# Kernel tuning notes

Hardware: AMD Instinct MI355X
Metric: run time of the kernel (lower is better)

The kernel has to match this reference:

```python
import jax, jax.numpy as jnp
import numpy as np

B, D, NB, BS = 32, 2048, 16, 512  # batch, dim_input=dim_output, n_blocks, block_size; NB*BS*BS == D*D


def setup_inputs() -> dict:
    key = jax.random.key(0)
    k1, k2, k3, k4, k5 = jax.random.split(key, 5)
    x = jax.random.normal(k1, (B, D), dtype=jnp.float32)
    gate_w = jax.random.normal(k2, (D, NB), dtype=jnp.float32) / np.sqrt(D)
    gate_b = jax.random.normal(k3, (NB,), dtype=jnp.float32) * 0.02
    weight = jax.random.normal(k4, (D, D), dtype=jnp.float32) / np.sqrt(D)  # kaiming-uniform-like scale
    bias = jax.random.normal(k5, (D,), dtype=jnp.float32) * (1.0 / np.sqrt(D))
    return {"x": x, "gate_w": gate_w, "gate_b": gate_b, "weight": weight, "bias": bias}


def reference(x, gate_w, gate_b, weight, bias):
    b = x.shape[0]
    k_drop = NB // 2
    # gate network: Linear -> Sigmoid
    g = jax.nn.sigmoid(x @ gate_w + gate_b)  # (b, NB)
    # zero out the k smallest gates per sample (topk largest=False, scatter 0)
    _, drop_idx = jax.lax.top_k(-g, k_drop)  # indices of smallest gates
    rows = jnp.arange(b)[:, None]
    g = g.at[rows, drop_idx].set(0.0)
    # broadcast gates over block-diagonal chunks of weight
    w0 = weight.reshape(NB, BS, BS)
    gw = (g[:, :, None, None] * w0).reshape(b, D, D)  # (b, dim_output, dim_input)
    # batched matvec + bias
    return jnp.einsum('bij,bj->bi', gw, x) + bias
```

## Files before the change

kernel.cpp:

```cpp
#include <hip/hip_runtime.h>
#include <hip/hip_bf16.h>


#define D_DIM 2048
#define B_DIM 32
#define NB_DIM 16
#define KSPLIT 8
#define KCHUNK (D_DIM / KSPLIT)

typedef __attribute__((ext_vector_type(4))) float f32x4;
typedef __attribute__((ext_vector_type(8))) float f32x8;
typedef __attribute__((ext_vector_type(8))) __bf16 bf16x8;

static __device__ __forceinline__ __bf16 f2bf(float f) {
    unsigned u = __builtin_bit_cast(unsigned, f);
    u += 0x7fffu + ((u >> 16) & 1u);
    unsigned short h = (unsigned short)(u >> 16);
    return __builtin_bit_cast(__bf16, h);
}

static __device__ __forceinline__ bf16x8 load_cvt8(const float* p) {
    const f32x8 v = *(const f32x8*)p;
    bf16x8 r;
#pragma unroll
    for (int i = 0; i < 8; ++i) r[i] = f2bf(v[i]);
    return r;
}

__global__ __launch_bounds__(256) void gates_kernel(
    const float* __restrict__ X,
    const float* __restrict__ GW,
    const float* __restrict__ GB,
    float* __restrict__ gates)
{
    __shared__ float red[NB_DIM][256];
    __shared__ float sg[NB_DIM];
    const int b = blockIdx.x;
    const int t = threadIdx.x;

    float acc[NB_DIM];
#pragma unroll
    for (int n = 0; n < NB_DIM; ++n) acc[n] = 0.f;

#pragma unroll
    for (int i = 0; i < D_DIM / 256; ++i) {
        const int c = t + i * 256;
        const float xv = X[b * D_DIM + c];
        const float* gw = GW + c * NB_DIM;
#pragma unroll
        for (int n = 0; n < NB_DIM; ++n) acc[n] += xv * gw[n];
    }
#pragma unroll
    for (int n = 0; n < NB_DIM; ++n) red[n][t] = acc[n];
    __syncthreads();
    for (int s = 128; s > 0; s >>= 1) {
        if (t < s) {
#pragma unroll
            for (int n = 0; n < NB_DIM; ++n) red[n][t] += red[n][t + s];
        }
        __syncthreads();
    }
    if (t < NB_DIM) {
        const float v = red[t][0] + GB[t];
        sg[t] = 1.f / (1.f + __expf(-v));
    }
    __syncthreads();
    if (t < NB_DIM) {
        const float g = sg[t];
        int rank = 0;
#pragma unroll
        for (int m = 0; m < NB_DIM; ++m) {
            const float gm = sg[m];
            if (gm < g || (gm == g && m < t)) rank++;
        }
        gates[b * NB_DIM + t] = (rank >= NB_DIM / 2) ? g : 0.f;
    }
}

__global__ __launch_bounds__(256) void main_gemm(
    const float* __restrict__ W,
    const float* __restrict__ X,
    float* __restrict__ part)
{
    const int bid  = blockIdx.x;
    const int ks   = bid & (KSPLIT - 1);
    const int rg   = bid >> 3;
    const int wave = threadIdx.x >> 6;
    const int lane = threadIdx.x & 63;
    const int l15  = lane & 15;
    const int q    = lane >> 4;

    const int r0 = rg * 64 + wave * 16;
    const int k0 = ks * KCHUNK;

    const float* arow = W + (size_t)(r0 + l15) * D_DIM + k0 + q * 8;
    const float* b0p  = X + (size_t)(l15)      * D_DIM + k0 + q * 8;
    const float* b1p  = X + (size_t)(l15 + 16) * D_DIM + k0 + q * 8;

    f32x4 acc0 = {0.f, 0.f, 0.f, 0.f};
    f32x4 acc1 = {0.f, 0.f, 0.f, 0.f};

#pragma unroll
    for (int kk = 0; kk < KCHUNK / 32; ++kk) {
        const bf16x8 av  = load_cvt8(arow + kk * 32);
        const bf16x8 bv0 = load_cvt8(b0p  + kk * 32);
        const bf16x8 bv1 = load_cvt8(b1p  + kk * 32);
        acc0 = __builtin_amdgcn_mfma_f32_16x16x32_bf16(av, bv0, acc0, 0, 0, 0);
        acc1 = __builtin_amdgcn_mfma_f32_16x16x32_bf16(av, bv1, acc1, 0, 0, 0);
    }

    float* p0 = part + (size_t)ks * (B_DIM * D_DIM) + (size_t)l15 * D_DIM        + r0 + q * 4;
    float* p1 = part + (size_t)ks * (B_DIM * D_DIM) + (size_t)(l15 + 16) * D_DIM + r0 + q * 4;
    *(f32x4*)p0 = acc0;
    *(f32x4*)p1 = acc1;
}

__global__ __launch_bounds__(256) void reduce_kernel(
    const float* __restrict__ part,
    const float* __restrict__ gates,
    const float* __restrict__ bias,
    float* __restrict__ out)
{
    const int t   = blockIdx.x * 256 + threadIdx.x;
    const int idx = t * 4;
    const int b   = idx >> 11;
    const int r   = idx & (D_DIM - 1);

    f32x4 s = {0.f, 0.f, 0.f, 0.f};
#pragma unroll
    for (int ks = 0; ks < KSPLIT; ++ks) {
        s += *(const f32x4*)(part + (size_t)ks * (B_DIM * D_DIM) + idx);
    }
    const float g = gates[b * NB_DIM + (r >> 7)];
    const f32x4 bi = *(const f32x4*)(bias + r);

    f32x4 y;
#pragma unroll
    for (int i = 0; i < 4; ++i) y[i] = g * s[i] + bi[i];
    *(f32x4*)(out + idx) = y;
}

extern "C" void kernel_launch(void* const* d_in, const int* in_sizes, int n_in,
                              void* d_out, int out_size, void* d_ws, size_t ws_size,
                              hipStream_t stream) {
    const float* x    = (const float*)d_in[0];
    const float* gw   = (const float*)d_in[1];
    const float* gb   = (const float*)d_in[2];
    const float* w    = (const float*)d_in[3];
    const float* bias = (const float*)d_in[4];
    float* out = (float*)d_out;

    float* part  = (float*)d_ws;
    float* gates = (float*)((char*)d_ws + (size_t)KSPLIT * B_DIM * D_DIM * sizeof(float));

    gates_kernel<<<B_DIM, 256, 0, stream>>>(x, gw, gb, gates);
    main_gemm<<<32 * KSPLIT, 256, 0, stream>>>(w, x, part);
    reduce_kernel<<<(B_DIM * D_DIM) / (256 * 4), 256, 0, stream>>>(part, gates, bias, out);
}
```

Baseline: 84.98 us.

## Replace split-K partial buffer and reduce kernel with gated atomic accumulation

Removes the separate reduction kernel and the partial-sum workspace. Bias initialisation of the output moves into the gates kernel as extra blocks, and the GEMM now scales each result by its gate and atomically adds it into the output. Blocks whose gate is zero skip the atomics. The split-K factor is doubled so more workgroups run, at the cost of more atomic traffic on the same output locations and nondeterministic summation order.

```diff
diff --git a/kernel.cpp b/kernel.cpp
--- a/kernel.cpp
+++ b/kernel.cpp
@@ -5,7 +5,7 @@
 #define D_DIM 2048
 #define B_DIM 32
 #define NB_DIM 16
-#define KSPLIT 8
+#define KSPLIT 16
 #define KCHUNK (D_DIM / KSPLIT)
 
 typedef __attribute__((ext_vector_type(4))) float f32x4;
@@ -27,16 +27,26 @@
     return r;
 }
 
-__global__ __launch_bounds__(256) void gates_kernel(
+__global__ __launch_bounds__(256) void prep_kernel(
     const float* __restrict__ X,
     const float* __restrict__ GW,
     const float* __restrict__ GB,
-    float* __restrict__ gates)
+    const float* __restrict__ bias,
+    float* __restrict__ gates,
+    float* __restrict__ out)
 {
+    const int t = threadIdx.x;
+
+    if (blockIdx.x >= B_DIM) {
+        const int idx4 = ((blockIdx.x - B_DIM) * 256 + t) * 4;
+        const int r = idx4 & (D_DIM - 1);
+        *(f32x4*)(out + idx4) = *(const f32x4*)(bias + r);
+        return;
+    }
+
     __shared__ float red[NB_DIM][256];
     __shared__ float sg[NB_DIM];
     const int b = blockIdx.x;
-    const int t = threadIdx.x;
 
     float acc[NB_DIM];
 #pragma unroll
@@ -77,14 +87,15 @@
     }
 }
 
-__global__ __launch_bounds__(256) void main_gemm(
+__global__ __launch_bounds__(256) void gemm_atomic(
     const float* __restrict__ W,
     const float* __restrict__ X,
-    float* __restrict__ part)
+    const float* __restrict__ gates,
+    float* __restrict__ out)
 {
     const int bid  = blockIdx.x;
     const int ks   = bid & (KSPLIT - 1);
-    const int rg   = bid >> 3;
+    const int rg   = bid >> 4;
     const int wave = threadIdx.x >> 6;
     const int lane = threadIdx.x & 63;
     const int l15  = lane & 15;
@@ -109,35 +120,21 @@
         acc1 = __builtin_amdgcn_mfma_f32_16x16x32_bf16(av, bv1, acc1, 0, 0, 0);
     }
 
-    float* p0 = part + (size_t)ks * (B_DIM * D_DIM) + (size_t)l15 * D_DIM        + r0 + q * 4;
-    float* p1 = part + (size_t)ks * (B_DIM * D_DIM) + (size_t)(l15 + 16) * D_DIM + r0 + q * 4;
-    *(f32x4*)p0 = acc0;
-    *(f32x4*)p1 = acc1;
-}
+    const int rbase = r0 + q * 4;
+    const int nblk  = rbase >> 7;
 
-__global__ __launch_bounds__(256) void reduce_kernel(
-    const float* __restrict__ part,
-    const float* __restrict__ gates,
-    const float* __restrict__ bias,
-    float* __restrict__ out)
-{
-    const int t   = blockIdx.x * 256 + threadIdx.x;
-    const int idx = t * 4;
-    const int b   = idx >> 11;
-    const int r   = idx & (D_DIM - 1);
-
-    f32x4 s = {0.f, 0.f, 0.f, 0.f};
+    const float g0 = gates[l15 * NB_DIM + nblk];
+    if (g0 != 0.f) {
+        float* o = out + (size_t)l15 * D_DIM + rbase;
 #pragma unroll
-    for (int ks = 0; ks < KSPLIT; ++ks) {
-        s += *(const f32x4*)(part + (size_t)ks * (B_DIM * D_DIM) + idx);
+        for (int i = 0; i < 4; ++i) atomicAdd(o + i, g0 * acc0[i]);
     }
-    const float g = gates[b * NB_DIM + (r >> 7)];
-    const f32x4 bi = *(const f32x4*)(bias + r);
-
-    f32x4 y;
+    const float g1 = gates[(l15 + 16) * NB_DIM + nblk];
+    if (g1 != 0.f) {
+        float* o = out + (size_t)(l15 + 16) * D_DIM + rbase;
 #pragma unroll
-    for (int i = 0; i < 4; ++i) y[i] = g * s[i] + bi[i];
-    *(f32x4*)(out + idx) = y;
+        for (int i = 0; i < 4; ++i) atomicAdd(o + i, g1 * acc1[i]);
+    }
 }
 
 extern "C" void kernel_launch(void* const* d_in, const int* in_sizes, int n_in,
@@ -150,10 +147,8 @@
     const float* bias = (const float*)d_in[4];
     float* out = (float*)d_out;
 
-    float* part  = (float*)d_ws;
-    float* gates = (float*)((char*)d_ws + (size_t)KSPLIT * B_DIM * D_DIM * sizeof(float));
+    float* gates = (float*)d_ws;
 
-    gates_kernel<<<B_DIM, 256, 0, stream>>>(x, gw, gb, gates);
-    main_gemm<<<32 * KSPLIT, 256, 0, stream>>>(w, x, part);
-    reduce_kernel<<<(B_DIM * D_DIM) / (256 * 4), 256, 0, stream>>>(part, gates, bias, out);
+    prep_kernel<<<B_DIM + 64, 256, 0, stream>>>(x, gw, gb, bias, gates, out);
+    gemm_atomic<<<32 * KSPLIT, 256, 0, stream>>>(w, x, gates, out);
 }
```

New measurement: 97.06 us. +14.2%, slower.
